# Optimization experiments

Measured on AMD Instinct MI355X. Metric: run time of the kernel, lower is better.

## Reference

```python
import jax, jax.numpy as jnp
import numpy as np

E, H, VOCAB = 32, 128, 32000
B, T = 32, 128


def _linear_params(key, out_f, in_f):
    kw, kb = jax.random.split(key)
    bound = 1.0 / np.sqrt(in_f)
    W = jax.random.uniform(kw, (out_f, in_f), jnp.float32, -bound, bound)
    b = jax.random.uniform(kb, (out_f,), jnp.float32, -bound, bound)
    return W, b


def setup_inputs() -> dict:
    key = jax.random.key(0)
    ks = jax.random.split(key, 10)
    x = jax.random.normal(ks[0], (B, T, E), jnp.float32)
    Wf, bWf = _linear_params(ks[1], H, E)
    Uf, bUf = _linear_params(ks[2], H, H)
    Wi, bWi = _linear_params(ks[3], H, E)
    Ui, bUi = _linear_params(ks[4], H, H)
    Wc, bWc = _linear_params(ks[5], H, E)
    Uc, bUc = _linear_params(ks[6], H, H)
    Wo, bWo = _linear_params(ks[7], H, E)
    Uo, bUo = _linear_params(ks[8], H, H)
    Vw, Vb = _linear_params(ks[9], VOCAB, H)
    return dict(x=x, Wf=Wf, bWf=bWf, Uf=Uf, bUf=bUf, Wi=Wi, bWi=bWi,
                Ui=Ui, bUi=bUi, Wc=Wc, bWc=bWc, Uc=Uc, bUc=bUc,
                Wo=Wo, bWo=bWo, Uo=Uo, bUo=bUo, Vw=Vw, Vb=Vb)


def _lstm_forward(x, Wf, bWf, Uf, bUf, Wi, bWi, Ui, bUi, Wc, bWc, Uc, bUc,
                  Wo, bWo, Uo, bUo, Vw, Vb):
    b = x.shape[0]
    # Precompute input-to-gate projections for all timesteps: [T, B, H] (time-major)
    xf = (jnp.einsum('bte,he->bth', x, Wf) + bWf).transpose(1, 0, 2)
    xi = (jnp.einsum('bte,he->bth', x, Wi) + bWi).transpose(1, 0, 2)
    xc = (jnp.einsum('bte,he->bth', x, Wc) + bWc).transpose(1, 0, 2)
    xo = (jnp.einsum('bte,he->bth', x, Wo) + bWo).transpose(1, 0, 2)

    h0 = jnp.zeros((b, H), x.dtype)
    c0 = jnp.zeros((b, H), x.dtype)

    def step(carry, xs):
        h, c = carry
        xf_t, xi_t, xc_t, xo_t = xs
        f = jax.nn.sigmoid(xf_t + h @ Uf.T + bUf)
        i = jax.nn.sigmoid(xi_t + h @ Ui.T + bUi)
        c_til = jnp.tanh(xc_t + h @ Uc.T + bUc)
        # Original module detaches the cell state before using it (self.ct = ct.detach())
        c_new = jax.lax.stop_gradient(f * c + i * c_til)
        o = jax.nn.sigmoid(xo_t + h @ Uo.T + bUo)
        h_new = o * jnp.tanh(c_new)
        out = h_new @ Vw.T + Vb  # [B, VOCAB]
        return (h_new, c_new), out

    (h_last, _), outs = jax.lax.scan(step, (h0, c0), (xf, xi, xc, xo))
    out_seq = outs.transpose(1, 0, 2)  # [B, T, VOCAB]
    return out_seq, h_last


def reference(x, Wf, bWf, Uf, bUf, Wi, bWi, Ui, bUi, Wc, bWc, Uc, bUc,
              Wo, bWo, Uo, bUo, Vw, Vb):
    return _lstm_forward(x, Wf, bWf, Uf, bUf, Wi, bWi, Ui, bUi, Wc, bWc,
                         Uc, bUc, Wo, bWo, Uo, bUo, Vw, Vb)
```

## Files before the change

### kernel.cpp

```cpp
#include <hip/hip_runtime.h>
#include <stdint.h>
#include <stddef.h>
#include <math.h>

#define E_ 32
#define H_ 128
#define V_ 32000
#define NB 32
#define NT 128
#define NCONS 224
#define NCHUNK 250
#define NX (NCHUNK - NCONS)
#define WSTEPS 16
#define NWIN (NT / WSTEPS)

typedef float f32x4 __attribute__((ext_vector_type(4)));
typedef short s16x8 __attribute__((ext_vector_type(8)));

__device__ inline unsigned short f2bf(float f) {
  uint32_t u = __float_as_uint(f);
  return (unsigned short)((u + 0x7FFFu + ((u >> 16) & 1u)) >> 16);
}

__device__ inline float dpp_xor1(float v) {
  return __int_as_float(__builtin_amdgcn_update_dpp(
      0, __float_as_int(v), 0xB1 , 0xF, 0xF, true));
}
__device__ inline float dpp_xor2(float v) {
  return __int_as_float(__builtin_amdgcn_update_dpp(
      0, __float_as_int(v), 0x4E , 0xF, 0xF, true));
}

__global__ void zero_cnt(int* cnt) {
  if (threadIdx.x < NWIN) cnt[threadIdx.x] = 0;
}

__global__ __launch_bounds__(512, 1)
void lstm_fused(const float* __restrict__ x,
                const float* __restrict__ Wf, const float* __restrict__ bWf,
                const float* __restrict__ Uf, const float* __restrict__ bUf,
                const float* __restrict__ Wi, const float* __restrict__ bWi,
                const float* __restrict__ Ui, const float* __restrict__ bUi,
                const float* __restrict__ Wc, const float* __restrict__ bWc,
                const float* __restrict__ Uc, const float* __restrict__ bUc,
                const float* __restrict__ Wo, const float* __restrict__ bWo,
                const float* __restrict__ Uo, const float* __restrict__ bUo,
                const float* __restrict__ Vw, const float* __restrict__ Vb,
                unsigned short* __restrict__ hbf,
                int* __restrict__ cnt,
                float* __restrict__ out,
                float* __restrict__ hlast)
{
  __shared__ __align__(16) unsigned char smem[81920];
  const int bid = blockIdx.x;
  const int tid = threadIdx.x;

  if (bid < NB) {
    float* xs = reinterpret_cast<float*>(smem);
    float* hd = reinterpret_cast<float*>(smem + 16384);

    const int q  = tid & 3;
    const int jj = tid >> 2;

    const float* WL[4]  = {Wf, Wi, Wc, Wo};
    const float* UL[4]  = {Uf, Ui, Uc, Uo};
    const float* bWL[4] = {bWf, bWi, bWc, bWo};
    const float* bUL[4] = {bUf, bUi, bUc, bUo};

    f32x4 wr_[4][2];
    f32x4 ur_[4][8];
    float bias_[4];
#pragma unroll
    for (int g = 0; g < 4; ++g) {
      const f32x4* Wp = reinterpret_cast<const f32x4*>(WL[g] + jj * E_ + q * 8);
      wr_[g][0] = Wp[0]; wr_[g][1] = Wp[1];
      const f32x4* Up = reinterpret_cast<const f32x4*>(UL[g] + jj * H_ + q * 32);
#pragma unroll
      for (int r = 0; r < 8; ++r) ur_[g][r] = Up[r];
      bias_[g] = bWL[g][jj] + bUL[g][jj];
    }

    for (int i = tid; i < NT * E_; i += 512) xs[i] = x[bid * (NT * E_) + i];
    if (tid < 144) hd[tid] = 0.f;
    float creg = 0.f;
    __syncthreads();

    for (int t = 0; t < NT; ++t) {
      const int cur = t & 1, nxt = cur ^ 1;
      const f32x4* hq = reinterpret_cast<const f32x4*>(hd + cur * 144 + q * 36);
      const f32x4* xq = reinterpret_cast<const f32x4*>(xs + t * E_ + q * 8);

      f32x4 p0 = {0.f,0.f,0.f,0.f}, p1 = p0, p2 = p0, p3 = p0;
#pragma unroll
      for (int r = 0; r < 2; ++r) {
        f32x4 xv = xq[r];
        p0 += wr_[0][r] * xv; p1 += wr_[1][r] * xv;
        p2 += wr_[2][r] * xv; p3 += wr_[3][r] * xv;
      }
#pragma unroll
      for (int r = 0; r < 8; ++r) {
        f32x4 hv = hq[r];
        p0 += ur_[0][r] * hv; p1 += ur_[1][r] * hv;
        p2 += ur_[2][r] * hv; p3 += ur_[3][r] * hv;
      }
      float s0 = (p0.x + p0.y) + (p0.z + p0.w);
      float s1 = (p1.x + p1.y) + (p1.z + p1.w);
      float s2 = (p2.x + p2.y) + (p2.z + p2.w);
      float s3 = (p3.x + p3.y) + (p3.z + p3.w);
      s0 += dpp_xor1(s0); s0 += dpp_xor2(s0);
      s1 += dpp_xor1(s1); s1 += dpp_xor2(s1);
      s2 += dpp_xor1(s2); s2 += dpp_xor2(s2);
      s3 += dpp_xor1(s3); s3 += dpp_xor2(s3);
      s0 += bias_[0]; s1 += bias_[1]; s2 += bias_[2]; s3 += bias_[3];

      float own = (q == 0) ? s0 : (q == 1) ? s1 : (q == 2) ? s2 : s3;
      float xin = (q == 2) ? own + own : own;
      float val = __builtin_amdgcn_rcpf(1.f + __expf(-xin));
      if (q == 2) val = 2.f * val - 1.f;
      float v1 = dpp_xor1(val);
      float v2 = dpp_xor2(val);
      float v3 = dpp_xor2(v1);
      float f_ = (q == 0) ? val : (q == 1) ? v1 : (q == 2) ? v2 : v3;
      float i_ = (q == 0) ? v1 : (q == 1) ? val : (q == 2) ? v3 : v2;
      float c_ = (q == 0) ? v2 : (q == 1) ? v3 : (q == 2) ? val : v1;
      float o_ = (q == 0) ? v3 : (q == 1) ? v2 : (q == 2) ? v1 : val;

      float cn = f_ * creg + i_ * c_;
      creg = cn;
      float hn = o_ * (2.f * __builtin_amdgcn_rcpf(1.f + __expf(-2.f * cn)) - 1.f);

      if (q == 0) {
        hd[nxt * 144 + jj + ((jj >> 5) << 2)] = hn;
        hbf[((size_t)t * NB + bid) * H_ + jj] = f2bf(hn);
        if (t == NT - 1) hlast[bid * H_ + jj] = hn;
      }
      __syncthreads();
      if ((t & (WSTEPS - 1)) == (WSTEPS - 1) && tid == 0)
        __hip_atomic_fetch_add(&cnt[t / WSTEPS], 1, __ATOMIC_RELEASE,
                               __HIP_MEMORY_SCOPE_AGENT);
    }
    return;
  }

  const int cid = bid - NB;
  unsigned char* vwo = smem;
  unsigned char* vwx = smem + 32768;
  unsigned char* hlb = smem + 65536;

  const int w = tid >> 6, lane = tid & 63;
  const int wr = w & 1, wc = w >> 1;
  const int l15 = lane & 15, lh = lane >> 4;

  for (int u = tid; u < 2048; u += 512) {
    int n = u >> 4, kc = u & 15;
    const f32x4* src = reinterpret_cast<const f32x4*>(
        Vw + ((size_t)(cid * 128 + n)) * H_ + kc * 8);
    f32x4 a = src[0], b = src[1];
    s16x8 o;
    o[0] = (short)f2bf(a.x); o[1] = (short)f2bf(a.y);
    o[2] = (short)f2bf(a.z); o[3] = (short)f2bf(a.w);
    o[4] = (short)f2bf(b.x); o[5] = (short)f2bf(b.y);
    o[6] = (short)f2bf(b.z); o[7] = (short)f2bf(b.w);
    *reinterpret_cast<s16x8*>(vwo + n * 256 + ((kc * 16) ^ ((n & 7) << 4))) = o;
  }
  float vbo0 = Vb[cid * 128 + wc * 32 + l15];
  float vbo1 = Vb[cid * 128 + wc * 32 + 16 + l15];
  const int hb_ = tid >> 4, hkc_ = tid & 15;
  const int hswz = hb_ * 256 + ((hkc_ * 16) ^ ((hb_ & 7) << 4));
  __syncthreads();

  for (int win = 0; win < NWIN; ++win) {
    if (tid == 0) {
      while (__hip_atomic_load(&cnt[win], __ATOMIC_RELAXED,
                               __HIP_MEMORY_SCOPE_AGENT) < NB)
        __builtin_amdgcn_s_sleep(8);
      (void)__hip_atomic_load(&cnt[win], __ATOMIC_ACQUIRE,
                              __HIP_MEMORY_SCOPE_AGENT);
    }
    __syncthreads();

    s16x8 hv = *reinterpret_cast<const s16x8*>(
        hbf + (size_t)(win * WSTEPS) * (NB * H_) + tid * 8);

    const int k = cid - NX * win;
    const bool duty = (k >= 0) && (k < NX);
    int chunk_x = NCONS + k;
    float vbx0 = 0.f, vbx1 = 0.f;
    if (duty) {
      for (int u = tid; u < 2048; u += 512) {
        int n = u >> 4, kc = u & 15;
        const f32x4* src = reinterpret_cast<const f32x4*>(
            Vw + ((size_t)(chunk_x * 128 + n)) * H_ + kc * 8);
        f32x4 a = src[0], b = src[1];
        s16x8 o;
        o[0] = (short)f2bf(a.x); o[1] = (short)f2bf(a.y);
        o[2] = (short)f2bf(a.z); o[3] = (short)f2bf(a.w);
        o[4] = (short)f2bf(b.x); o[5] = (short)f2bf(b.y);
        o[6] = (short)f2bf(b.z); o[7] = (short)f2bf(b.w);
        *reinterpret_cast<s16x8*>(vwx + n * 256 + ((kc * 16) ^ ((n & 7) << 4))) = o;
      }
      vbx0 = Vb[chunk_x * 128 + wc * 32 + l15];
      vbx1 = Vb[chunk_x * 128 + wc * 32 + 16 + l15];
    }

    for (int tt = 0; tt < WSTEPS; ++tt) {
      const int t = win * WSTEPS + tt;
      unsigned char* hcur = hlb + (tt & 1) * 8192;
      *reinterpret_cast<s16x8*>(hcur + hswz) = hv;
      if (tt < WSTEPS - 1)
        hv = *reinterpret_cast<const s16x8*>(
            hbf + (size_t)(t + 1) * (NB * H_) + tid * 8);
      __syncthreads();

      s16x8 af[4];
      const int ra = wr * 16 + l15;
#pragma unroll
      for (int kt = 0; kt < 4; ++kt)
        af[kt] = *reinterpret_cast<const s16x8*>(
            hcur + ra * 256 + ((kt * 64 + lh * 16) ^ ((ra & 7) << 4)));

      const int rb = wc * 32 + l15;
      {
        f32x4 acc0 = {0.f,0.f,0.f,0.f}, acc1 = acc0;
#pragma unroll
        for (int kt = 0; kt < 4; ++kt) {
          s16x8 b0 = *reinterpret_cast<const s16x8*>(
              vwo + rb * 256 + ((kt * 64 + lh * 16) ^ ((rb & 7) << 4)));
          s16x8 b1 = *reinterpret_cast<const s16x8*>(
              vwo + (rb + 16) * 256 + ((kt * 64 + lh * 16) ^ (((rb + 16) & 7) << 4)));
          acc0 = __builtin_amdgcn_mfma_f32_16x16x32_bf16(af[kt], b0, acc0, 0, 0, 0);
          acc1 = __builtin_amdgcn_mfma_f32_16x16x32_bf16(af[kt], b1, acc1, 0, 0, 0);
        }
        const int colbase = cid * 128 + wc * 32;
#pragma unroll
        for (int i = 0; i < 4; ++i) {
          int b = wr * 16 + lh * 4 + i;
          float* orow = out + ((size_t)b * NT + t) * V_ + colbase;
          orow[l15]      = acc0[i] + vbo0;
          orow[16 + l15] = acc1[i] + vbo1;
        }
      }
      if (duty) {
        f32x4 acc0 = {0.f,0.f,0.f,0.f}, acc1 = acc0;
#pragma unroll
        for (int kt = 0; kt < 4; ++kt) {
          s16x8 b0 = *reinterpret_cast<const s16x8*>(
              vwx + rb * 256 + ((kt * 64 + lh * 16) ^ ((rb & 7) << 4)));
          s16x8 b1 = *reinterpret_cast<const s16x8*>(
              vwx + (rb + 16) * 256 + ((kt * 64 + lh * 16) ^ (((rb + 16) & 7) << 4)));
          acc0 = __builtin_amdgcn_mfma_f32_16x16x32_bf16(af[kt], b0, acc0, 0, 0, 0);
          acc1 = __builtin_amdgcn_mfma_f32_16x16x32_bf16(af[kt], b1, acc1, 0, 0, 0);
        }
        const int colbase = chunk_x * 128 + wc * 32;
#pragma unroll
        for (int i = 0; i < 4; ++i) {
          int b = wr * 16 + lh * 4 + i;
          float* orow = out + ((size_t)b * NT + t) * V_ + colbase;
          orow[l15]      = acc0[i] + vbx0;
          orow[16 + l15] = acc1[i] + vbx1;
        }
      }
    }
  }
}

extern "C" void kernel_launch(void* const* d_in, const int* in_sizes, int n_in,
                              void* d_out, int out_size, void* d_ws, size_t ws_size,
                              hipStream_t stream) {
  const float* x   = (const float*)d_in[0];
  const float* Wf  = (const float*)d_in[1];
  const float* bWf = (const float*)d_in[2];
  const float* Uf  = (const float*)d_in[3];
  const float* bUf = (const float*)d_in[4];
  const float* Wi  = (const float*)d_in[5];
  const float* bWi = (const float*)d_in[6];
  const float* Ui  = (const float*)d_in[7];
  const float* bUi = (const float*)d_in[8];
  const float* Wc  = (const float*)d_in[9];
  const float* bWc = (const float*)d_in[10];
  const float* Uc  = (const float*)d_in[11];
  const float* bUc = (const float*)d_in[12];
  const float* Wo  = (const float*)d_in[13];
  const float* bWo = (const float*)d_in[14];
  const float* Uo  = (const float*)d_in[15];
  const float* bUo = (const float*)d_in[16];
  const float* Vw  = (const float*)d_in[17];
  const float* Vb  = (const float*)d_in[18];
  float* out = (float*)d_out;

  unsigned short* hbf = (unsigned short*)d_ws;
  int* cnt = (int*)((char*)d_ws + (1u << 20));
  float* hlast = out + (size_t)NB * NT * V_;

  hipLaunchKernelGGL(zero_cnt, dim3(1), dim3(64), 0, stream, cnt);
  hipLaunchKernelGGL(lstm_fused, dim3(256), dim3(512), 0, stream,
                     x, Wf, bWf, Uf, bUf, Wi, bWi, Ui, bUi, Wc, bWc, Uc, bUc,
                     Wo, bWo, Uo, bUo, Vw, Vb, hbf, cnt, out, hlast);
}
```

Before: 166.3 us.

## Give each consumer block 256 vocab columns with register-resident weights

Consumer blocks now each own a fixed 256-column slice of the output projection, so there are 125 consumers instead of 224 plus rotating extra-duty chunks, and the grid shrinks to 157 blocks. The bf16 weight fragments are loaded once into registers rather than re-read from LDS every timestep, and the per-window extra chunk conversion is removed. This balances work evenly and cuts LDS traffic, but each block now does twice the MFMA and store work per step with fewer blocks, and register pressure rises (64 VGPRs of weights).

```diff
diff --git a/kernel.cpp b/kernel.cpp
--- a/kernel.cpp
+++ b/kernel.cpp
@@ -8,9 +8,7 @@
 #define V_ 32000
 #define NB 32
 #define NT 128
-#define NCONS 224
-#define NCHUNK 250
-#define NX (NCHUNK - NCONS)
+#define NCONS 125
 #define WSTEPS 16
 #define NWIN (NT / WSTEPS)
 
@@ -24,11 +22,11 @@
 
 __device__ inline float dpp_xor1(float v) {
   return __int_as_float(__builtin_amdgcn_update_dpp(
-      0, __float_as_int(v), 0xB1 , 0xF, 0xF, true));
+      0, __float_as_int(v), 0xB1, 0xF, 0xF, true));
 }
 __device__ inline float dpp_xor2(float v) {
   return __int_as_float(__builtin_amdgcn_update_dpp(
-      0, __float_as_int(v), 0x4E , 0xF, 0xF, true));
+      0, __float_as_int(v), 0x4E, 0xF, 0xF, true));
 }
 
 __global__ void zero_cnt(int* cnt) {
@@ -144,17 +142,16 @@
 
   const int cid = bid - NB;
   unsigned char* vwo = smem;
-  unsigned char* vwx = smem + 32768;
   unsigned char* hlb = smem + 65536;
 
   const int w = tid >> 6, lane = tid & 63;
   const int wr = w & 1, wc = w >> 1;
   const int l15 = lane & 15, lh = lane >> 4;
 
-  for (int u = tid; u < 2048; u += 512) {
+  for (int u = tid; u < 4096; u += 512) {
     int n = u >> 4, kc = u & 15;
     const f32x4* src = reinterpret_cast<const f32x4*>(
-        Vw + ((size_t)(cid * 128 + n)) * H_ + kc * 8);
+        Vw + ((size_t)(cid * 256 + n)) * H_ + kc * 8);
     f32x4 a = src[0], b = src[1];
     s16x8 o;
     o[0] = (short)f2bf(a.x); o[1] = (short)f2bf(a.y);
@@ -163,11 +160,23 @@
     o[6] = (short)f2bf(b.z); o[7] = (short)f2bf(b.w);
     *reinterpret_cast<s16x8*>(vwo + n * 256 + ((kc * 16) ^ ((n & 7) << 4))) = o;
   }
-  float vbo0 = Vb[cid * 128 + wc * 32 + l15];
-  float vbo1 = Vb[cid * 128 + wc * 32 + 16 + l15];
+  float vb[4];
+#pragma unroll
+  for (int g = 0; g < 4; ++g)
+    vb[g] = Vb[cid * 256 + wc * 64 + g * 16 + l15];
   const int hb_ = tid >> 4, hkc_ = tid & 15;
   const int hswz = hb_ * 256 + ((hkc_ * 16) ^ ((hb_ & 7) << 4));
   __syncthreads();
+
+  s16x8 bO[4][4];
+#pragma unroll
+  for (int g = 0; g < 4; ++g) {
+    const int rbg = wc * 64 + g * 16 + l15;
+#pragma unroll
+    for (int kt = 0; kt < 4; ++kt)
+      bO[g][kt] = *reinterpret_cast<const s16x8*>(
+          vwo + rbg * 256 + ((kt * 64 + lh * 16) ^ ((rbg & 7) << 4)));
+  }
 
   for (int win = 0; win < NWIN; ++win) {
     if (tid == 0) {
@@ -181,27 +190,6 @@
 
     s16x8 hv = *reinterpret_cast<const s16x8*>(
         hbf + (size_t)(win * WSTEPS) * (NB * H_) + tid * 8);
-
-    const int k = cid - NX * win;
-    const bool duty = (k >= 0) && (k < NX);
-    int chunk_x = NCONS + k;
-    float vbx0 = 0.f, vbx1 = 0.f;
-    if (duty) {
-      for (int u = tid; u < 2048; u += 512) {
-        int n = u >> 4, kc = u & 15;
-        const f32x4* src = reinterpret_cast<const f32x4*>(
-            Vw + ((size_t)(chunk_x * 128 + n)) * H_ + kc * 8);
-        f32x4 a = src[0], b = src[1];
-        s16x8 o;
-        o[0] = (short)f2bf(a.x); o[1] = (short)f2bf(a.y);
-        o[2] = (short)f2bf(a.z); o[3] = (short)f2bf(a.w);
-        o[4] = (short)f2bf(b.x); o[5] = (short)f2bf(b.y);
-        o[6] = (short)f2bf(b.z); o[7] = (short)f2bf(b.w);
-        *reinterpret_cast<s16x8*>(vwx + n * 256 + ((kc * 16) ^ ((n & 7) << 4))) = o;
-      }
-      vbx0 = Vb[chunk_x * 128 + wc * 32 + l15];
-      vbx1 = Vb[chunk_x * 128 + wc * 32 + 16 + l15];
-    }
 
     for (int tt = 0; tt < WSTEPS; ++tt) {
       const int t = win * WSTEPS + tt;
@@ -219,46 +207,23 @@
         af[kt] = *reinterpret_cast<const s16x8*>(
             hcur + ra * 256 + ((kt * 64 + lh * 16) ^ ((ra & 7) << 4)));
 
-      const int rb = wc * 32 + l15;
-      {
-        f32x4 acc0 = {0.f,0.f,0.f,0.f}, acc1 = acc0;
-#pragma unroll
-        for (int kt = 0; kt < 4; ++kt) {
-          s16x8 b0 = *reinterpret_cast<const s16x8*>(
-              vwo + rb * 256 + ((kt * 64 + lh * 16) ^ ((rb & 7) << 4)));
-          s16x8 b1 = *reinterpret_cast<const s16x8*>(
-              vwo + (rb + 16) * 256 + ((kt * 64 + lh * 16) ^ (((rb + 16) & 7) << 4)));
-          acc0 = __builtin_amdgcn_mfma_f32_16x16x32_bf16(af[kt], b0, acc0, 0, 0, 0);
-          acc1 = __builtin_amdgcn_mfma_f32_16x16x32_bf16(af[kt], b1, acc1, 0, 0, 0);
-        }
-        const int colbase = cid * 128 + wc * 32;
-#pragma unroll
-        for (int i = 0; i < 4; ++i) {
-          int b = wr * 16 + lh * 4 + i;
-          float* orow = out + ((size_t)b * NT + t) * V_ + colbase;
-          orow[l15]      = acc0[i] + vbo0;
-          orow[16 + l15] = acc1[i] + vbo1;
-        }
-      }
-      if (duty) {
-        f32x4 acc0 = {0.f,0.f,0.f,0.f}, acc1 = acc0;
-#pragma unroll
-        for (int kt = 0; kt < 4; ++kt) {
-          s16x8 b0 = *reinterpret_cast<const s16x8*>(
-              vwx + rb * 256 + ((kt * 64 + lh * 16) ^ ((rb & 7) << 4)));
-          s16x8 b1 = *reinterpret_cast<const s16x8*>(
-              vwx + (rb + 16) * 256 + ((kt * 64 + lh * 16) ^ (((rb + 16) & 7) << 4)));
-          acc0 = __builtin_amdgcn_mfma_f32_16x16x32_bf16(af[kt], b0, acc0, 0, 0, 0);
-          acc1 = __builtin_amdgcn_mfma_f32_16x16x32_bf16(af[kt], b1, acc1, 0, 0, 0);
-        }
-        const int colbase = chunk_x * 128 + wc * 32;
-#pragma unroll
-        for (int i = 0; i < 4; ++i) {
-          int b = wr * 16 + lh * 4 + i;
-          float* orow = out + ((size_t)b * NT + t) * V_ + colbase;
-          orow[l15]      = acc0[i] + vbx0;
-          orow[16 + l15] = acc1[i] + vbx1;
-        }
+      f32x4 acc[4];
+#pragma unroll
+      for (int g = 0; g < 4; ++g) acc[g] = (f32x4){0.f, 0.f, 0.f, 0.f};
+#pragma unroll
+      for (int kt = 0; kt < 4; ++kt) {
+#pragma unroll
+        for (int g = 0; g < 4; ++g)
+          acc[g] = __builtin_amdgcn_mfma_f32_16x16x32_bf16(af[kt], bO[g][kt], acc[g], 0, 0, 0);
+      }
+      const int colbase = cid * 256 + wc * 64;
+#pragma unroll
+      for (int i = 0; i < 4; ++i) {
+        int b = wr * 16 + lh * 4 + i;
+        float* orow = out + ((size_t)b * NT + t) * V_ + colbase;
+#pragma unroll
+        for (int g = 0; g < 4; ++g)
+          orow[g * 16 + l15] = acc[g][i] + vb[g];
       }
     }
   }
@@ -293,7 +258,7 @@
   float* hlast = out + (size_t)NB * NT * V_;
 
   hipLaunchKernelGGL(zero_cnt, dim3(1), dim3(64), 0, stream, cnt);
-  hipLaunchKernelGGL(lstm_fused, dim3(256), dim3(512), 0, stream,
+  hipLaunchKernelGGL(lstm_fused, dim3(NB + NCONS), dim3(512), 0, stream,
                      x, Wf, bWf, Uf, bUf, Wi, bWi, Ui, bUi, Wc, bWc, Uc, bUc,
                      Wo, bWo, Uo, bUo, Vw, Vb, hbf, cnt, out, hlast);
 }
```

New measurement: 183.6 us. +10.4%, slower.
